# Performance work log

Measured on AMD Instinct MI355X. Metric: run time of the kernel, lower is better.

Reference implementation:

```python
import jax, jax.numpy as jnp
import numpy as np

B, S, I, H = 512, 1024, 20, 64  # batch, seq_len, input_size, hidden_size


def setup_inputs() -> dict:
    key = jax.random.key(0)
    ks = jax.random.split(key, 12)
    # one-hot protein sequences with variable true lengths (padding is all-zero rows)
    lengths = jax.random.randint(ks[0], (B,), 100, S + 1)
    tokens = jax.random.randint(ks[1], (B, S), 0, I)
    valid = (jnp.arange(S)[None, :] < lengths[:, None]).astype(jnp.float32)
    input1 = jax.nn.one_hot(tokens, I, dtype=jnp.float32) * valid[:, :, None]

    def nrm(k, shape, s=0.05):
        return jax.random.normal(k, shape, jnp.float32) * s

    return {
        'input1': input1,
        'W_ih_f': nrm(ks[2], (4 * H, I)), 'W_hh_f': nrm(ks[3], (4 * H, H)), 'b_f': nrm(ks[4], (4 * H,)),
        'W_ih_b': nrm(ks[5], (4 * H, I)), 'W_hh_b': nrm(ks[6], (4 * H, H)), 'b_b': nrm(ks[7], (4 * H,)),
        'conv1_w': nrm(ks[8], (20, 20), 1.0),           # blosum pssm: [out_c=20, kernel_w=20]
        'conv2_w': nrm(ks[9], (100, 4, 20)), 'conv2_b': nrm(ks[9], (100,)),
        'fc1_w': nrm(ks[10], (64, 228)), 'fc1_b': nrm(ks[10], (64,)),
        'fc2_w': nrm(ks[11], (2, 64)), 'fc2_b': nrm(ks[11], (2,)),
    }


def _lstm_final(x, W_ih, W_hh, b):
    # x: [B,S,I] -> final hidden state [B,H]; torch gate order i,f,g,o
    xs = jnp.einsum('bsi,gi->sbg', x, W_ih) + b  # [S,B,4H]

    def step(carry, gx):
        h, c = carry
        g = gx + h @ W_hh.T
        i, f, gg, o = jnp.split(g, 4, axis=-1)
        c = jax.nn.sigmoid(f) * c + jax.nn.sigmoid(i) * jnp.tanh(gg)
        h = jax.nn.sigmoid(o) * jnp.tanh(c)
        return (h, c), None

    init = (jnp.zeros((x.shape[0], H), x.dtype), jnp.zeros((x.shape[0], H), x.dtype))
    (h, _), _ = jax.lax.scan(step, init, xs)
    return h


def reference(input1, W_ih_f, W_hh_f, b_f, W_ih_b, W_hh_b, b_b,
              conv1_w, conv2_w, conv2_b, fc1_w, fc1_b, fc2_w, fc2_b):
    # BiLSTM: final hidden state of each direction (dropout is identity in eval)
    h_fw = _lstm_final(input1, W_ih_f, W_hh_f, b_f)
    h_bw = _lstm_final(input1[:, ::-1, :], W_ih_b, W_hh_b, b_b)
    lstm_output = jnp.concatenate([h_fw, h_bw], axis=1)  # [B,128]

    # conv1: kernel (1,20) spans the full width -> per-position linear map. [B,20,S]
    c1 = jnp.einsum('bsj,cj->bcs', input1, conv1_w)
    # faithful torch.reshape (B,20,S,1)->(B,S,1,20): row-major reinterpretation
    c1 = c1.reshape(input1.shape[0], S, 20)  # [B,S,20]

    # ragged 4-bin segment mean over the first width[i]=4*(len[i]//4) positions
    lens = jnp.sum(input1, axis=(1, 2)).astype(jnp.int32)
    bw = jnp.floor(lens / 4).astype(jnp.int32)
    width = bw * 4
    pos = jnp.arange(S)[None, :]                       # [1,S]
    bin_idx = pos // bw[:, None]                       # [B,S]
    valid = pos < width[:, None]                       # [B,S]
    mask = ((bin_idx[:, None, :] == jnp.arange(4)[None, :, None]) & valid[:, None, :]).astype(c1.dtype)  # [B,4,S]
    avblock = jnp.einsum('bks,bsc->bkc', mask, c1) / bw.astype(c1.dtype)[:, None, None]  # [B,4,20]

    # conv2: kernel (4,20) spans the whole avblock -> one dot per out channel
    c2 = jnp.einsum('bkc,okc->bo', avblock, conv2_w) + conv2_b  # [B,100]
    c2 = jax.nn.relu(c2)

    merged = jnp.concatenate([lstm_output, c2], axis=1)  # [B,228]
    fc1 = merged @ fc1_w.T + fc1_b
    fc2 = fc1 @ fc2_w.T + fc2_b
    return jax.nn.softmax(fc2, axis=1)
```

## Files before the change

### kernel.cpp

```cpp
#include <hip/hip_runtime.h>
#include <hip/hip_bf16.h>

#define BB 512
#define SS 1024
#define NI 20
#define HH 64
#define NG 256
#define MB4 4
#define PAD 80
#define TSTR 257

typedef unsigned short u16;
typedef unsigned int u32;
typedef unsigned long long u64;
typedef _Float16 f16;
typedef f16 f16x8 __attribute__((ext_vector_type(8)));
typedef float f32x4 __attribute__((ext_vector_type(4)));

#define LOG2E 1.4426950408889634f

__device__ __forceinline__ float bf2f(u16 b) { return __uint_as_float(((u32)b) << 16); }
__device__ __forceinline__ float ldw(const void* p, int idx, int mode) {
  return mode ? bf2f(((const u16*)p)[idx]) : ((const float*)p)[idx];
}
__device__ __forceinline__ float frcp(float x) { return __builtin_amdgcn_rcpf(x); }
__device__ __forceinline__ float fexp2(float x) { return __builtin_amdgcn_exp2f(x); }

__global__ __launch_bounds__(256)
void lstm_kernel(const void* in1,
                 const void* Wih_f, const void* Whh_f, const void* b_f,
                 const void* Wih_b, const void* Whh_b, const void* b_b,
                 short* toks_g, int* lens, float* hout) {
  int bx = blockIdx.x;
  int dir = bx >> 7;
  int b0 = (bx & 127) * MB4;
  int t = threadIdx.x;
  int w = t >> 6, lane = t & 63, l = lane & 15, q = lane >> 4;
  int bsel = l >> 2;

  __shared__ __align__(16) float table[21 * TSTR];
  __shared__ __align__(16) f16 hbuf[2][MB4][PAD];
  __shared__ short tok_s[SS * MB4];
  __shared__ u64 red[256];
  __shared__ int mode_sh;

  if (t == 0) mode_sh = 1;
  __syncthreads();
  {
    float v = bf2f(((const u16*)b_f)[t]);
    if (!(fabsf(v) < 1000.0f)) atomicAnd(&mode_sh, 0);
  }
  __syncthreads();
  int mode = mode_sh;
  const void* Wih = dir ? Wih_b : Wih_f;
  const void* Whh = dir ? Whh_b : Whh_f;
  const void* bv  = dir ? b_b   : b_f;

  u64 cnt = 0;
  for (int m = 0; m < MB4; ++m) {
    if (mode) {
      u32* st = (u32*)table;
      for (int k0 = 0; k0 < 4; ++k0) {
        const u32* src = (const u32*)in1 + ((size_t)(b0 + m) * SS + k0 * 256) * 10;
#pragma unroll
        for (int i = 0; i < 10; ++i) st[t + i * 256] = src[t + i * 256];
        __syncthreads();
        const u32* row = st + t * 10;
        int tok = -1;
#pragma unroll
        for (int ww = 0; ww < 10; ++ww) {
          u32 u = row[ww];
          if (u & 0xFFFFu) tok = 2 * ww;
          if (u >> 16)     tok = 2 * ww + 1;
        }
        tok_s[(k0 * 256 + t) * MB4 + m] = (short)(tok + 1);
        if (dir == 0) toks_g[(size_t)(b0 + m) * SS + k0 * 256 + t] = (short)tok;
        cnt += (u64)(tok >= 0) << (16 * m);
        __syncthreads();
      }
    } else {
      float4* st = (float4*)table;
      for (int k0 = 0; k0 < 4; ++k0) {
        const float4* src = (const float4*)((const float*)in1 + ((size_t)(b0 + m) * SS + k0 * 256) * 20);
#pragma unroll
        for (int i = 0; i < 5; ++i) st[t + i * 256] = src[t + i * 256];
        __syncthreads();
        const float* row = (const float*)table + t * 20;
        int tok = -1;
#pragma unroll
        for (int ww = 0; ww < 20; ++ww)
          if (row[ww] != 0.f) tok = ww;
        tok_s[(k0 * 256 + t) * MB4 + m] = (short)(tok + 1);
        if (dir == 0) toks_g[(size_t)(b0 + m) * SS + k0 * 256 + t] = (short)tok;
        cnt += (u64)(tok >= 0) << (16 * m);
        __syncthreads();
      }
    }
  }
  red[t] = cnt;
  __syncthreads();
  for (int stp = 128; stp > 0; stp >>= 1) {
    if (t < stp) red[t] += red[t + stp];
    __syncthreads();
  }
  if (dir == 0 && t < MB4)
    lens[b0 + t] = (int)((red[0] >> (16 * t)) & 0xFFFFull);
  __syncthreads();

  for (int idx = t; idx < 21 * 256; idx += 256) {
    int r = idx >> 8, g = idx & 255;
    float scl = ((g >> 6) == 2) ? (2.f * LOG2E) : (-LOG2E);
    float v = ldw(bv, g, mode);
    if (r > 0) v += ldw(Wih, g * NI + (r - 1), mode);
    table[r * TSTR + g] = scl * v;
  }
  f16x8 Bf[4][2];
#pragma unroll
  for (int tt = 0; tt < 4; ++tt) {
    float scl = (tt == 2) ? (2.f * LOG2E) : (-LOG2E);
    int g = 64 * tt + 16 * w + l;
#pragma unroll
    for (int kc = 0; kc < 2; ++kc) {
      f16x8 v;
#pragma unroll
      for (int j = 0; j < 8; ++j)
        v[j] = (f16)(scl * ldw(Whh, g * HH + kc * 32 + q * 8 + j, mode));
      Bf[tt][kc] = v;
    }
  }
  for (int idx = t; idx < 2 * MB4 * PAD; idx += 256)
    ((f16*)hbuf)[idx] = (f16)0.f;
  __syncthreads();

  float c_st = 0.f, hlast = 0.f;
  int jj = 16 * w + l;
  int tbase = 16 * w + l;

  float wxc[4];
  {
    int pos0 = dir ? (SS - 1) : 0;
    int base = (int)tok_s[pos0 * MB4 + q] * TSTR + tbase;
    wxc[0] = table[base];       wxc[1] = table[base + 64];
    wxc[2] = table[base + 128]; wxc[3] = table[base + 192];
  }
  int tok1;
  {
    int pos1 = dir ? (SS - 2) : 1;
    tok1 = (int)tok_s[pos1 * MB4 + q];
  }

#pragma unroll 2
  for (int s = 0; s < SS; ++s) {
    int p = s & 1;
    f16x8 a0 = *(const f16x8*)&hbuf[p][bsel][q * 8];
    f16x8 a1 = *(const f16x8*)&hbuf[p][bsel][32 + q * 8];
    float wxn[4];
    {
      int base = tok1 * TSTR + tbase;
      wxn[0] = table[base];       wxn[1] = table[base + 64];
      wxn[2] = table[base + 128]; wxn[3] = table[base + 192];
    }
    {
      int pos2 = (dir ? (SS - 3 - s) : (s + 2)) & (SS - 1);
      tok1 = (int)tok_s[pos2 * MB4 + q];
    }

    f32x4 acc[4];
#pragma unroll
    for (int tt = 0; tt < 4; ++tt) {
      f32x4 ci = {wxc[tt], wxc[tt], wxc[tt], wxc[tt]};
      acc[tt] = __builtin_amdgcn_mfma_f32_16x16x32_f16(a0, Bf[tt][0], ci, 0, 0, 0);
    }
#pragma unroll
    for (int tt = 0; tt < 4; ++tt)
      acc[tt] = __builtin_amdgcn_mfma_f32_16x16x32_f16(a1, Bf[tt][1], acc[tt], 0, 0, 0);

    {
      float Ei = fexp2(acc[0][0]);
      float Ef = fexp2(acc[1][0]);
      float G  = fexp2(acc[2][0]);
      float Eo = fexp2(acc[3][0]);
      float Ei1 = Ei + 1.f, Ef1 = Ef + 1.f, G1 = G + 1.f, Gm = G - 1.f;
      float t1 = Ei1 * G1;
      float num = fmaf(c_st, t1, Gm * Ef1);
      float cv = num * frcp(t1 * Ef1);
      c_st = cv;
      float C = fexp2((2.f * LOG2E) * cv);
      float hv = (C - 1.f) * frcp((Eo + 1.f) * (C + 1.f));
      hlast = hv;
      hbuf[p ^ 1][q][jj] = (f16)hv;
    }
    __syncthreads();
    wxc[0] = wxn[0]; wxc[1] = wxn[1]; wxc[2] = wxn[2]; wxc[3] = wxn[3];
  }
  hout[(b0 + q) * 128 + dir * 64 + jj] = hlast;
}

__global__ __launch_bounds__(256)
void head_kernel(const void* conv1_w, const void* conv2_w, const void* conv2_b,
                 const void* fc1_w, const void* fc1_b,
                 const void* fc2_w, const void* fc2_b,
                 const void* bvec, const short* toks, const int* lens,
                 const float* hout, void* out) {
  int b = blockIdx.x;
  int t = threadIdx.x;
  __shared__ float c1w[400];
  __shared__ short tok_s[SS];
  __shared__ float pav[3][80];
  __shared__ float avg[80];
  __shared__ float cpart[2][100];
  __shared__ float merged[228];
  __shared__ float fpart[4][64];
  __shared__ float fc1v[64];
  __shared__ float f2p[2][64];
  __shared__ int mode_sh;

  if (t == 0) mode_sh = 1;
  __syncthreads();
  {
    float v = bf2f(((const u16*)bvec)[t]);
    if (!(fabsf(v) < 1000.0f)) atomicAnd(&mode_sh, 0);
  }
  __syncthreads();
  int mode = mode_sh;

  for (int i = t; i < 400; i += 256) c1w[i] = ldw(conv1_w, i, mode);
  for (int s = t; s < SS; s += 256) tok_s[s] = toks[(size_t)b * SS + s];
  __syncthreads();

  int len = lens[b];
  int bw = len >> 2;
  if (t < 240) {
    int seg = t / 80;
    int u = t - seg * 80;
    int k = u / 20, cc = u % 20;
    int base = k * bw;
    int s0 = base + (seg * bw) / 3;
    int s1 = base + ((seg + 1) * bw) / 3;
    float p0 = 0.f, p1 = 0.f, p2 = 0.f, p3 = 0.f;
    int s = s0;
    for (; s + 4 <= s1; s += 4) {
      int f0 = s * 20 + cc, f1 = f0 + 20, f2 = f0 + 40, f3 = f0 + 60;
      int tk0 = tok_s[f0 & 1023];
      int tk1 = tok_s[f1 & 1023];
      int tk2 = tok_s[f2 & 1023];
      int tk3 = tok_s[f3 & 1023];
      if (tk0 >= 0) p0 += c1w[(f0 >> 10) * 20 + tk0];
      if (tk1 >= 0) p1 += c1w[(f1 >> 10) * 20 + tk1];
      if (tk2 >= 0) p2 += c1w[(f2 >> 10) * 20 + tk2];
      if (tk3 >= 0) p3 += c1w[(f3 >> 10) * 20 + tk3];
    }
    for (; s < s1; ++s) {
      int f = s * 20 + cc;
      int tk = tok_s[f & 1023];
      if (tk >= 0) p0 += c1w[(f >> 10) * 20 + tk];
    }
    pav[seg][u] = (p0 + p1) + (p2 + p3);
  }
  __syncthreads();
  if (t < 80) avg[t] = (pav[0][t] + pav[1][t] + pav[2][t]) / (float)bw;
  __syncthreads();

  if (t < 200) {
    int half = t / 100, o = t - half * 100;
    float dot = 0.f;
    int q0 = half * 40;
#pragma unroll 8
    for (int q = q0; q < q0 + 40; ++q)
      dot = fmaf(avg[q], ldw(conv2_w, o * 80 + q, mode), dot);
    cpart[half][o] = dot;
  }
  if (t < 128) merged[t] = hout[b * 128 + t];
  __syncthreads();
  if (t < 100) {
    float dot = cpart[0][t] + cpart[1][t] + ldw(conv2_b, t, mode);
    merged[128 + t] = dot > 0.f ? dot : 0.f;
  }
  __syncthreads();

  {
    int o = t & 63, ch = t >> 6;
    float v = 0.f;
    int m0 = ch * 57;
#pragma unroll 8
    for (int m = m0; m < m0 + 57; ++m)
      v = fmaf(merged[m], ldw(fc1_w, o * 228 + m, mode), v);
    fpart[ch][o] = v;
  }
  __syncthreads();
  if (t < 64)
    fc1v[t] = fpart[0][t] + fpart[1][t] + fpart[2][t] + fpart[3][t] + ldw(fc1_b, t, mode);
  __syncthreads();

  if (t < 128) {
    int o = t >> 6, m = t & 63;
    f2p[o][m] = fc1v[m] * ldw(fc2_w, o * 64 + m, mode);
  }
  __syncthreads();
  for (int stp = 32; stp > 0; stp >>= 1) {
    if (t < 128) {
      int o = t >> 6, m = t & 63;
      if (m < stp) f2p[o][m] += f2p[o][m + stp];
    }
    __syncthreads();
  }
  if (t == 0) {
    float x0 = f2p[0][0] + ldw(fc2_b, 0, mode);
    float x1 = f2p[1][0] + ldw(fc2_b, 1, mode);
    float mx = fmaxf(x0, x1);
    float e0 = fexp2(LOG2E * (x0 - mx)), e1 = fexp2(LOG2E * (x1 - mx));
    float inv = frcp(e0 + e1);
    if (mode) {
      ((__hip_bfloat16*)out)[b * 2 + 0] = __float2bfloat16(e0 * inv);
      ((__hip_bfloat16*)out)[b * 2 + 1] = __float2bfloat16(e1 * inv);
    } else {
      ((float*)out)[b * 2 + 0] = e0 * inv;
      ((float*)out)[b * 2 + 1] = e1 * inv;
    }
  }
}

extern "C" void kernel_launch(void* const* d_in, const int* in_sizes, int n_in,
                              void* d_out, int out_size, void* d_ws, size_t ws_size,
                              hipStream_t stream) {
  (void)in_sizes; (void)n_in; (void)out_size; (void)ws_size;
  char* ws = (char*)d_ws;
  int*   lens = (int*)(ws + 256);
  short* toks = (short*)(ws + 256 + 2048);
  float* hout = (float*)(ws + 256 + 2048 + (size_t)BB * SS * sizeof(short));

  lstm_kernel<<<256, 256, 0, stream>>>(d_in[0],
                                       d_in[1], d_in[2], d_in[3],
                                       d_in[4], d_in[5], d_in[6],
                                       toks, lens, hout);
  head_kernel<<<BB, 256, 0, stream>>>(d_in[7], d_in[8], d_in[9],
                                      d_in[10], d_in[11], d_in[12], d_in[13],
                                      d_in[3], toks, lens, hout, d_out);
}
```

Baseline: 391.3 us.

## Split LSTM work to one batch row per block with 1024 blocks

The LSTM kernel now gives each block a single batch row and direction instead of four rows, and launches four times as many blocks. Several independent recurrences can then share a CU and hide each other's per-step latency from MFMA, transcendental ops and barriers. In exchange, the 16-row MFMA tiles and the per-lane gate math now repeat the same row four times. That is four times the instructions for the same useful work, and each block rebuilds its own gate lookup table.

Measured after the change: 702.2 us. +79.4%, slower.

```diff
diff --git a/kernel.cpp b/kernel.cpp
--- a/kernel.cpp
+++ b/kernel.cpp
@@ -6,7 +6,6 @@
 #define NI 20
 #define HH 64
 #define NG 256
-#define MB4 4
 #define PAD 80
 #define TSTR 257
 
@@ -32,16 +31,15 @@
                  const void* Wih_b, const void* Whh_b, const void* b_b,
                  short* toks_g, int* lens, float* hout) {
   int bx = blockIdx.x;
-  int dir = bx >> 7;
-  int b0 = (bx & 127) * MB4;
+  int dir = bx >> 9;
+  int b0 = bx & 511;
   int t = threadIdx.x;
   int w = t >> 6, lane = t & 63, l = lane & 15, q = lane >> 4;
-  int bsel = l >> 2;
 
   __shared__ __align__(16) float table[21 * TSTR];
-  __shared__ __align__(16) f16 hbuf[2][MB4][PAD];
-  __shared__ short tok_s[SS * MB4];
-  __shared__ u64 red[256];
+  __shared__ __align__(16) f16 hbuf[2][PAD];
+  __shared__ short tok_s[SS];
+  __shared__ int red[256];
   __shared__ int mode_sh;
 
   if (t == 0) mode_sh = 1;
@@ -56,45 +54,43 @@
   const void* Whh = dir ? Whh_b : Whh_f;
   const void* bv  = dir ? b_b   : b_f;
 
-  u64 cnt = 0;
-  for (int m = 0; m < MB4; ++m) {
-    if (mode) {
-      u32* st = (u32*)table;
-      for (int k0 = 0; k0 < 4; ++k0) {
-        const u32* src = (const u32*)in1 + ((size_t)(b0 + m) * SS + k0 * 256) * 10;
-#pragma unroll
-        for (int i = 0; i < 10; ++i) st[t + i * 256] = src[t + i * 256];
-        __syncthreads();
-        const u32* row = st + t * 10;
-        int tok = -1;
-#pragma unroll
-        for (int ww = 0; ww < 10; ++ww) {
-          u32 u = row[ww];
-          if (u & 0xFFFFu) tok = 2 * ww;
-          if (u >> 16)     tok = 2 * ww + 1;
-        }
-        tok_s[(k0 * 256 + t) * MB4 + m] = (short)(tok + 1);
-        if (dir == 0) toks_g[(size_t)(b0 + m) * SS + k0 * 256 + t] = (short)tok;
-        cnt += (u64)(tok >= 0) << (16 * m);
-        __syncthreads();
+  int cnt = 0;
+  if (mode) {
+    u32* st = (u32*)table;
+    for (int k0 = 0; k0 < 4; ++k0) {
+      const u32* src = (const u32*)in1 + ((size_t)b0 * SS + k0 * 256) * 10;
+#pragma unroll
+      for (int i = 0; i < 10; ++i) st[t + i * 256] = src[t + i * 256];
+      __syncthreads();
+      const u32* row = st + t * 10;
+      int tok = -1;
+#pragma unroll
+      for (int ww = 0; ww < 10; ++ww) {
+        u32 u = row[ww];
+        if (u & 0xFFFFu) tok = 2 * ww;
+        if (u >> 16)     tok = 2 * ww + 1;
       }
-    } else {
-      float4* st = (float4*)table;
-      for (int k0 = 0; k0 < 4; ++k0) {
-        const float4* src = (const float4*)((const float*)in1 + ((size_t)(b0 + m) * SS + k0 * 256) * 20);
-#pragma unroll
-        for (int i = 0; i < 5; ++i) st[t + i * 256] = src[t + i * 256];
-        __syncthreads();
-        const float* row = (const float*)table + t * 20;
-        int tok = -1;
-#pragma unroll
-        for (int ww = 0; ww < 20; ++ww)
-          if (row[ww] != 0.f) tok = ww;
-        tok_s[(k0 * 256 + t) * MB4 + m] = (short)(tok + 1);
-        if (dir == 0) toks_g[(size_t)(b0 + m) * SS + k0 * 256 + t] = (short)tok;
-        cnt += (u64)(tok >= 0) << (16 * m);
-        __syncthreads();
-      }
+      tok_s[k0 * 256 + t] = (short)(tok + 1);
+      if (dir == 0) toks_g[(size_t)b0 * SS + k0 * 256 + t] = (short)tok;
+      cnt += (tok >= 0);
+      __syncthreads();
+    }
+  } else {
+    float4* st = (float4*)table;
+    for (int k0 = 0; k0 < 4; ++k0) {
+      const float4* src = (const float4*)((const float*)in1 + ((size_t)b0 * SS + k0 * 256) * 20);
+#pragma unroll
+      for (int i = 0; i < 5; ++i) st[t + i * 256] = src[t + i * 256];
+      __syncthreads();
+      const float* row = (const float*)table + t * 20;
+      int tok = -1;
+#pragma unroll
+      for (int ww = 0; ww < 20; ++ww)
+        if (row[ww] != 0.f) tok = ww;
+      tok_s[k0 * 256 + t] = (short)(tok + 1);
+      if (dir == 0) toks_g[(size_t)b0 * SS + k0 * 256 + t] = (short)tok;
+      cnt += (tok >= 0);
+      __syncthreads();
     }
   }
   red[t] = cnt;
@@ -103,8 +99,7 @@
     if (t < stp) red[t] += red[t + stp];
     __syncthreads();
   }
-  if (dir == 0 && t < MB4)
-    lens[b0 + t] = (int)((red[0] >> (16 * t)) & 0xFFFFull);
+  if (dir == 0 && t == 0) lens[b0] = red[0];
   __syncthreads();
 
   for (int idx = t; idx < 21 * 256; idx += 256) {
@@ -128,41 +123,40 @@
       Bf[tt][kc] = v;
     }
   }
-  for (int idx = t; idx < 2 * MB4 * PAD; idx += 256)
+  for (int idx = t; idx < 2 * PAD; idx += 256)
     ((f16*)hbuf)[idx] = (f16)0.f;
   __syncthreads();
 
   float c_st = 0.f, hlast = 0.f;
   int jj = 16 * w + l;
-  int tbase = 16 * w + l;
 
   float wxc[4];
   {
     int pos0 = dir ? (SS - 1) : 0;
-    int base = (int)tok_s[pos0 * MB4 + q] * TSTR + tbase;
+    int base = (int)tok_s[pos0] * TSTR + jj;
     wxc[0] = table[base];       wxc[1] = table[base + 64];
     wxc[2] = table[base + 128]; wxc[3] = table[base + 192];
   }
   int tok1;
   {
     int pos1 = dir ? (SS - 2) : 1;
-    tok1 = (int)tok_s[pos1 * MB4 + q];
+    tok1 = (int)tok_s[pos1];
   }
 
 #pragma unroll 2
   for (int s = 0; s < SS; ++s) {
     int p = s & 1;
-    f16x8 a0 = *(const f16x8*)&hbuf[p][bsel][q * 8];
-    f16x8 a1 = *(const f16x8*)&hbuf[p][bsel][32 + q * 8];
+    f16x8 a0 = *(const f16x8*)&hbuf[p][q * 8];
+    f16x8 a1 = *(const f16x8*)&hbuf[p][32 + q * 8];
     float wxn[4];
     {
-      int base = tok1 * TSTR + tbase;
+      int base = tok1 * TSTR + jj;
       wxn[0] = table[base];       wxn[1] = table[base + 64];
       wxn[2] = table[base + 128]; wxn[3] = table[base + 192];
     }
     {
       int pos2 = (dir ? (SS - 3 - s) : (s + 2)) & (SS - 1);
-      tok1 = (int)tok_s[pos2 * MB4 + q];
+      tok1 = (int)tok_s[pos2];
     }
 
     f32x4 acc[4];
@@ -188,12 +182,12 @@
       float C = fexp2((2.f * LOG2E) * cv);
       float hv = (C - 1.f) * frcp((Eo + 1.f) * (C + 1.f));
       hlast = hv;
-      hbuf[p ^ 1][q][jj] = (f16)hv;
+      if (q == 0) hbuf[p ^ 1][jj] = (f16)hv;
     }
     __syncthreads();
     wxc[0] = wxn[0]; wxc[1] = wxn[1]; wxc[2] = wxn[2]; wxc[3] = wxn[3];
   }
-  hout[(b0 + q) * 128 + dir * 64 + jj] = hlast;
+  if (q == 0) hout[b0 * 128 + dir * 64 + jj] = hlast;
 }
 
 __global__ __launch_bounds__(256)
@@ -329,10 +323,10 @@
   short* toks = (short*)(ws + 256 + 2048);
   float* hout = (float*)(ws + 256 + 2048 + (size_t)BB * SS * sizeof(short));
 
-  lstm_kernel<<<256, 256, 0, stream>>>(d_in[0],
-                                       d_in[1], d_in[2], d_in[3],
-                                       d_in[4], d_in[5], d_in[6],
-                                       toks, lens, hout);
+  lstm_kernel<<<1024, 256, 0, stream>>>(d_in[0],
+                                        d_in[1], d_in[2], d_in[3],
+                                        d_in[4], d_in[5], d_in[6],
+                                        toks, lens, hout);
   head_kernel<<<BB, 256, 0, stream>>>(d_in[7], d_in[8], d_in[9],
                                       d_in[10], d_in[11], d_in[12], d_in[13],
                                       d_in[3], toks, lens, hout, d_out);
```
